# Kernel tuning notes

Measured on AMD Instinct MI355X. Metric: run time of the kernel, lower is better.

## Reference

```python
import jax, jax.numpy as jnp
import numpy as np

B, C_IN, N_NODES = 128, 64, 1024
N_TRIPLES = 3 * (N_NODES - 1)  # node 0 is the shared zero vector


def _btc(x, idx, w, b):
    # x: [B, C, N]; idx: [B, 3M]; w: [O, C, 3]; b: [O]
    Bv, C, _ = x.shape
    T = idx.shape[1]
    g = jnp.take_along_axis(x, jnp.broadcast_to(idx[:, None, :], (Bv, C, T)), axis=2)
    g = g.reshape(Bv, C, T // 3, 3)  # stride-3 kernel-3 conv == per-triple contraction
    out = jnp.einsum('bcnk,ock->bon', g, w) + b[None, :, None]
    zero = jnp.zeros((Bv, out.shape[1], 1), dtype=out.dtype)
    return jnp.concatenate([zero, out], axis=2)  # re-prepend zero node -> [B, O, N]


def _tln(x):
    mean = jnp.mean(x, axis=(1, 2), keepdims=True)
    std = jnp.std(x, axis=(1, 2), ddof=1, keepdims=True)  # torch.std is unbiased
    return (x - mean) / (std + 1e-5)


def _tower(x, idx, p):
    x = jax.nn.leaky_relu(_tln(_btc(x, idx, p['w_conv1'], p['b_conv1'])), 0.01)
    x = jax.nn.leaky_relu(_tln(_btc(x, idx, p['w_conv2'], p['b_conv2'])), 0.01)
    x = _tln(_btc(x, idx, p['w_conv3'], p['b_conv3']))
    x = jnp.max(x, axis=2)  # DynamicPooling -> [B, 64]
    x = jax.nn.leaky_relu(x @ p['w_fc1'].T + p['b_fc1'], 0.01)
    return x @ p['w_fc2'].T + p['b_fc2']  # [B, 1]  (Dropout is identity at eval)


def setup_inputs() -> dict:
    key = jax.random.key(0)
    ks = jax.random.split(key, 12)
    s = 0.05
    return {
        'data1': jax.random.normal(ks[0], (B, C_IN, N_NODES), jnp.float32),
        'idx1': jax.random.randint(ks[1], (B, N_TRIPLES, 1), 0, N_NODES, dtype=jnp.int64)
                if jax.config.jax_enable_x64 else
                jax.random.randint(ks[1], (B, N_TRIPLES, 1), 0, N_NODES).astype(jnp.int32),
        'data2': jax.random.normal(ks[2], (B, C_IN, N_NODES), jnp.float32),
        'idx2': jax.random.randint(ks[3], (B, N_TRIPLES, 1), 0, N_NODES).astype(jnp.int32),
        'w_conv1': jax.random.normal(ks[4], (256, C_IN, 3), jnp.float32) * s,
        'b_conv1': jnp.zeros((256,), jnp.float32),
        'w_conv2': jax.random.normal(ks[5], (128, 256, 3), jnp.float32) * s,
        'b_conv2': jnp.zeros((128,), jnp.float32),
        'w_conv3': jax.random.normal(ks[6], (64, 128, 3), jnp.float32) * s,
        'b_conv3': jnp.zeros((64,), jnp.float32),
        'w_fc1': jax.random.normal(ks[7], (32, 64), jnp.float32) * s,
        'b_fc1': jnp.zeros((32,), jnp.float32),
        'w_fc2': jax.random.normal(ks[8], (1, 32), jnp.float32) * s,
        'b_fc2': jnp.zeros((1,), jnp.float32),
    }


def reference(data1, idx1, data2, idx2,
              w_conv1, b_conv1, w_conv2, b_conv2, w_conv3, b_conv3,
              w_fc1, b_fc1, w_fc2, b_fc2):
    p = dict(w_conv1=w_conv1, b_conv1=b_conv1, w_conv2=w_conv2, b_conv2=b_conv2,
             w_conv3=w_conv3, b_conv3=b_conv3, w_fc1=w_fc1, b_fc1=b_fc1,
             w_fc2=w_fc2, b_fc2=b_fc2)
    y1 = _tower(data1, idx1[..., 0], p)
    y2 = _tower(data2, idx2[..., 0], p)
    return jnp.squeeze(jax.nn.sigmoid(y1 - y2), axis=1)  # [B]
```

## Files before the change

### kernel.cpp

```cpp
#include <hip/hip_runtime.h>
#include <math.h>

typedef __attribute__((ext_vector_type(8))) short short8;
typedef __attribute__((ext_vector_type(4))) float f32x4;
typedef __attribute__((ext_vector_type(2))) float f32x2;

#define LRELU(x) ((x) > 0.0f ? (x) : 0.01f * (x))

struct __align__(4) Int3 { int x, y, z; };

__device__ __forceinline__ unsigned short f2bf(float f) {
    unsigned int u = __float_as_uint(f);
    return (unsigned short)((u + 0x7FFFu + ((u >> 16) & 1u)) >> 16);
}
__device__ __forceinline__ unsigned int pack_bf16_pair(float lo, float hi) {
    unsigned int ul = __float_as_uint(lo) + 0x8000u;
    unsigned int uh = __float_as_uint(hi) + 0x8000u;
    return (ul >> 16) | (uh & 0xFFFF0000u);
}
__device__ __forceinline__ float2 stats_from(const float* sums, int b, float count) {
    float s = sums[2 * b], q = sums[2 * b + 1];
    float mean = s / count;
    float var = (q - s * s / count) / (count - 1.0f);
    var = fmaxf(var, 0.0f);
    return make_float2(mean, 1.0f / (sqrtf(var) + 1e-5f));
}
__device__ __forceinline__ void atomicMaxF(float* a, float v) {
    if (v >= 0.0f) atomicMax((int*)a, __float_as_int(v));
    else           atomicMin((unsigned int*)a, __float_as_uint(v));
}
__device__ __forceinline__ unsigned int fp8x4_nact(unsigned int u, float a, float c) {
    f32x2 lo = __builtin_amdgcn_cvt_pk_f32_fp8(u, false);
    f32x2 hi = __builtin_amdgcn_cvt_pk_f32_fp8(u, true);
    lo = lo * a + c; hi = hi * a + c;
    f32x2 ml = lo * 0.01f, mh = hi * 0.01f;
    lo = __builtin_elementwise_max(lo, ml);
    hi = __builtin_elementwise_max(hi, mh);
    int r = __builtin_amdgcn_cvt_pk_fp8_f32(lo.x, lo.y, 0, false);
    r = __builtin_amdgcn_cvt_pk_fp8_f32(hi.x, hi.y, r, true);
    return (unsigned int)r;
}

template <int MT, int WM>
__device__ __forceinline__ void mfma_step(const unsigned short* wt, const unsigned short* gt,
                                          f32x4 (&acc)[MT][4],
                                          int wo, int wn, int quad, int l15, int blkid)
{
#pragma unroll
    for (int st = 0; st < 2; ++st) {
        short8 af[MT], bfv[4];
        const int qb = st * 4 + quad;
#pragma unroll
        for (int i = 0; i < MT; i++) {
            const int orow = wo * WM + i * 16 + l15;
            af[i] = *(const short8*)&wt[orow * 64 + ((qb ^ blkid) << 3)];
        }
#pragma unroll
        for (int t = 0; t < 4; t++) {
            const int nrow = wn * 64 + t * 16 + l15;
            bfv[t] = *(const short8*)&gt[nrow * 64 + ((qb ^ blkid) << 3)];
        }
#pragma unroll
        for (int i = 0; i < MT; i++)
#pragma unroll
            for (int t = 0; t < 4; t++)
                acc[i][t] = __builtin_amdgcn_mfma_f32_16x16x32_bf16(
                    af[i], bfv[t], acc[i][t], 0, 0, 0);
    }
}

__global__ void prep_all(const float* __restrict__ w1, unsigned short* __restrict__ wq1,
                         const float* __restrict__ w2, unsigned char* __restrict__ wq2,
                         const float* __restrict__ w3, unsigned char* __restrict__ wq3)
{
    const int tid = blockIdx.x * blockDim.x + threadIdx.x;
    const int stride = gridDim.x * blockDim.x;
    for (int i = tid; i < 256 * 192; i += stride) {
        int o = i / 192, kp = i - o * 192;
        int j = kp >> 6, c = kp & 63;
        wq1[i] = f2bf(w1[(o * 64 + c) * 3 + j]);
    }
    for (int i = tid; i < (128 * 768) >> 2; i += stride) {
        const int e0 = i << 2;
        const int o = e0 / 768, kp0 = e0 - o * 768;
        const int j = kp0 >> 8, c0 = kp0 & 255;
        const float* src = &w2[(o * 256 + c0) * 3 + j];
        float f0 = src[0], f1 = src[3], f2 = src[6], f3 = src[9];
        int r = __builtin_amdgcn_cvt_pk_fp8_f32(f0, f1, 0, false);
        r = __builtin_amdgcn_cvt_pk_fp8_f32(f2, f3, r, true);
        *(unsigned int*)&wq2[e0] = (unsigned int)r;
    }
    for (int i = tid; i < (64 * 384) >> 2; i += stride) {
        const int e0 = i << 2;
        const int o = e0 / 384, kp0 = e0 - o * 384;
        const int j = kp0 >> 7, c0 = kp0 & 127;
        const float* src = &w3[(o * 128 + c0) * 3 + j];
        float f0 = src[0], f1 = src[3], f2 = src[6], f3 = src[9];
        int r = __builtin_amdgcn_cvt_pk_fp8_f32(f0, f1, 0, false);
        r = __builtin_amdgcn_cvt_pk_fp8_f32(f2, f3, r, true);
        *(unsigned int*)&wq3[e0] = (unsigned int)r;
    }
}

__global__ __launch_bounds__(256) void transpose_in(const float* __restrict__ inA,
                                                    const float* __restrict__ inB,
                                                    unsigned short* __restrict__ xT,
                                                    float* __restrict__ sums,
                                                    unsigned int* __restrict__ pmax)
{
    const int b = blockIdx.y, n0 = blockIdx.x * 64;
    const float* in = (b >= 128 ? inB : inA) + ((size_t)(b & 127) * 64) * 1024;
    const int tid = threadIdx.x;
    if (blockIdx.x == 0 && blockIdx.y == 0) {
        const int nBv = gridDim.y;
        for (int i = tid; i < 3 * nBv * 2; i += 256) sums[i] = 0.0f;
        for (int i = tid; i < nBv * 64; i += 256) pmax[i] = 0xFFFFFFFFu;
    }
    __shared__ float tile[64][65];
    const int nn = tid & 63, cw = tid >> 6;
#pragma unroll
    for (int i = 0; i < 16; i++) {
        int c = i * 4 + cw;
        tile[c][nn] = in[(size_t)c * 1024 + n0 + nn];
    }
    __syncthreads();
    const int n = tid >> 2, cp = (tid & 3) * 16;
    unsigned int pk[8];
#pragma unroll
    for (int i = 0; i < 8; i++) {
        unsigned short lo = f2bf(tile[cp + 2 * i][n]);
        unsigned short hi = f2bf(tile[cp + 2 * i + 1][n]);
        pk[i] = (unsigned int)lo | ((unsigned int)hi << 16);
    }
    unsigned short* dst = xT + ((size_t)b * 1024 + n0 + n) * 64 + cp;
    uint4 v0 = {pk[0], pk[1], pk[2], pk[3]};
    uint4 v1 = {pk[4], pk[5], pk[6], pk[7]};
    *(uint4*)dst = v0;
    *(uint4*)(dst + 8) = v1;
}

__global__ __launch_bounds__(256) void norm_act_fp8(unsigned char* __restrict__ a,
                                                    const float* __restrict__ sums,
                                                    float count, int u4PerB)
{
    const int b = blockIdx.y;
    float2 st = stats_from(sums, b, count);
    const float na = st.y, nc = -st.x * st.y;
    uint4* p = (uint4*)a + (size_t)b * u4PerB;
    for (int idx = blockIdx.x * 256 + threadIdx.x; idx < u4PerB; idx += gridDim.x * 256) {
        uint4 v = p[idx];
        v.x = fp8x4_nact(v.x, na, nc);
        v.y = fp8x4_nact(v.y, na, nc);
        v.z = fp8x4_nact(v.z, na, nc);
        v.w = fp8x4_nact(v.w, na, nc);
        p[idx] = v;
    }
}

__global__ __launch_bounds__(256, 3) void conv1_mfma(
    const unsigned short* __restrict__ xT,
    const int* __restrict__ idxA,
    const int* __restrict__ idxB,
    const unsigned short* __restrict__ wq,
    const float* __restrict__ bias,
    unsigned char* __restrict__ out,
    float* __restrict__ sums)
{
    const int b   = blockIdx.x;
    const int o0  = blockIdx.y * 128;
    const int nt0 = blockIdx.z << 7;
    const int tid = threadIdx.x;
    const int lane = tid & 63, wave = tid >> 6;
    const int wo = wave & 1, wn = wave >> 1;
    const int quad = lane >> 4, l15 = lane & 15;
    const int blkid = lane & 7;

    __shared__ __align__(16) unsigned short wt[128 * 64];
    __shared__ __align__(16) unsigned short gt[128 * 64];

    f32x4 acc[4][4];
#pragma unroll
    for (int i = 0; i < 4; i++)
#pragma unroll
        for (int t = 0; t < 4; t++) acc[i][t] = (f32x4){0.f, 0.f, 0.f, 0.f};

    const unsigned short* xTb = xT + (((size_t)b) << 10) * 64;
    const int* idxb = (b >= 128 ? idxB : idxA) + (size_t)(b & 127) * 3069;

    const int gr = tid >> 1, gh = tid & 1;
    int s0, s1, s2;
    {
        int n = nt0 + gr;
        int t0 = (n == 0) ? 0 : (n - 1);
        const Int3 sv = *(const Int3*)&idxb[3 * t0];
        s0 = sv.x; s1 = sv.y; s2 = sv.z;
    }
    const int wr = tid >> 1, wseg = tid & 1;
    const unsigned short* wrow = wq + (size_t)(o0 + wr) * 192 + wseg * 32;
    const int gswz = gr & 7, wswz = wr & 7;

    uint4 g0A, g1A, g2A, g3A;
    uint4 g0B, g1B, g2B, g3B;

#define LOADC(S, KC) {                                                           \
        const int src_ = ((KC) == 0) ? s0 : (((KC) == 1) ? s1 : s2);             \
        const uint4* gp_ = (const uint4*)(xTb + (size_t)src_ * 64 + gh * 32);    \
        g0##S = gp_[0]; g1##S = gp_[1]; g2##S = gp_[2]; g3##S = gp_[3];          \
    }

#define STAGE(S, KC) {                                                           \
        const uint4* wp_ = (const uint4*)(wrow + ((KC) << 6));                   \
        uint4 wv0 = wp_[0], wv1 = wp_[1], wv2 = wp_[2], wv3 = wp_[3];            \
        *(uint4*)&gt[gr * 64 + (((gh << 2) | 0) ^ gswz) * 8] = g0##S;            \
        *(uint4*)&gt[gr * 64 + (((gh << 2) | 1) ^ gswz) * 8] = g1##S;            \
        *(uint4*)&gt[gr * 64 + (((gh << 2) | 2) ^ gswz) * 8] = g2##S;            \
        *(uint4*)&gt[gr * 64 + (((gh << 2) | 3) ^ gswz) * 8] = g3##S;            \
        *(uint4*)&wt[wr * 64 + ((wseg * 4 + 0) ^ wswz) * 8] = wv0;               \
        *(uint4*)&wt[wr * 64 + ((wseg * 4 + 1) ^ wswz) * 8] = wv1;               \
        *(uint4*)&wt[wr * 64 + ((wseg * 4 + 2) ^ wswz) * 8] = wv2;               \
        *(uint4*)&wt[wr * 64 + ((wseg * 4 + 3) ^ wswz) * 8] = wv3;               \
    }

    LOADC(A, 0);
    LOADC(B, 1);
    int kc = 0;
    for (; kc + 2 <= 3; kc += 2) {
        if (kc) __syncthreads();
        STAGE(A, kc);
        if (kc + 2 < 3) LOADC(A, kc + 2);
        __syncthreads();
        mfma_step<4, 64>(wt, gt, acc, wo, wn, quad, l15, blkid);
        __syncthreads();
        STAGE(B, kc + 1);
        __syncthreads();
        mfma_step<4, 64>(wt, gt, acc, wo, wn, quad, l15, blkid);
    }
    {
        __syncthreads();
        STAGE(A, 2);
        __syncthreads();
        mfma_step<4, 64>(wt, gt, acc, wo, wn, quad, l15, blkid);
    }
#undef LOADC
#undef STAGE

    __syncthreads();
    unsigned char* eb = (unsigned char*)gt;
    float lsum = 0.f, lsq = 0.f;
#pragma unroll
    for (int i = 0; i < 4; i++) {
        const int obl = wo * 64 + i * 16 + quad * 4;
        const float4 bv = *(const float4*)(bias + o0 + obl);
#pragma unroll
        for (int t = 0; t < 4; t++) {
            const int nl = wn * 64 + t * 16 + l15;
            float v0 = acc[i][t][0] + bv.x;
            float v1 = acc[i][t][1] + bv.y;
            float v2 = acc[i][t][2] + bv.z;
            float v3 = acc[i][t][3] + bv.w;
            if (nt0 + nl == 0) { v0 = v1 = v2 = v3 = 0.f; }
            lsum += v0 + v1 + v2 + v3;
            lsq  += v0 * v0 + v1 * v1 + v2 * v2 + v3 * v3;
            int r = __builtin_amdgcn_cvt_pk_fp8_f32(v0, v1, 0, false);
            r = __builtin_amdgcn_cvt_pk_fp8_f32(v2, v3, r, true);
            *(unsigned int*)&eb[nl * 128 + (obl ^ ((nl & 7) << 4))] = (unsigned int)r;
        }
    }
#pragma unroll
    for (int off = 32; off > 0; off >>= 1) {
        lsum += __shfl_down(lsum, off);
        lsq  += __shfl_down(lsq, off);
    }
    float* red = (float*)wt;
    if (lane == 0) { red[wave] = lsum; red[4 + wave] = lsq; }
    __syncthreads();
#pragma unroll
    for (int c = 0; c < 4; ++c) {
        const int ch = c * 256 + tid;
        const int row = ch >> 3, off = (ch & 7) << 4;
        uint4 v = *(const uint4*)&eb[row * 128 + (off ^ ((row & 7) << 4))];
        *(uint4*)&out[((size_t)b * 1024 + nt0 + row) * 256 + o0 + off] = v;
    }
    if (tid == 0) {
        atomicAdd(&sums[2 * b + 0], red[0] + red[1] + red[2] + red[3]);
        atomicAdd(&sums[2 * b + 1], red[4] + red[5] + red[6] + red[7]);
    }
}

__global__ __launch_bounds__(256, 3) void conv2_fp8(
    const unsigned char* __restrict__ a1,
    const int* __restrict__ idxA,
    const int* __restrict__ idxB,
    const unsigned char* __restrict__ wq8,
    const float* __restrict__ bias,
    unsigned char* __restrict__ out,
    float* __restrict__ sums)
{
    const int b   = blockIdx.x;
    const int nt0 = blockIdx.z << 7;
    const int tid = threadIdx.x;
    const int lane = tid & 63, wave = tid >> 6;
    const int wo = wave & 1, wn = wave >> 1;
    const int quad = lane >> 4, l15 = lane & 15;
    const int blkid = lane & 7;

    __shared__ __align__(16) unsigned char wt8[128 * 128];
    __shared__ __align__(16) unsigned char gt8[128 * 128];

    f32x4 acc[4][4];
#pragma unroll
    for (int i = 0; i < 4; i++)
#pragma unroll
        for (int t = 0; t < 4; t++) acc[i][t] = (f32x4){0.f, 0.f, 0.f, 0.f};

    const unsigned char* xb = a1 + (((size_t)b) << 10) * 256;
    const int* idxb = (b >= 128 ? idxB : idxA) + (size_t)(b & 127) * 3069;

    const int gr = tid >> 1, gh = tid & 1;
    int si0, si1, si2;
    {
        int n = nt0 + gr;
        int t0 = (n == 0) ? 0 : (n - 1);
        const Int3 sv = *(const Int3*)&idxb[3 * t0];
        si0 = sv.x; si1 = sv.y; si2 = sv.z;
    }
    const unsigned char* wrow = wq8 + (size_t)gr * 768 + gh * 64;
    const int swz = gr & 7;

    uint4 g0A, g1A, g2A, g3A;
    uint4 g0B, g1B, g2B, g3B;

#define LOADC2(S, KC) {                                                          \
        const int j_  = (KC) >> 1;                                               \
        const int c0_ = ((KC) & 1) << 7;                                         \
        const int src_ = (j_ == 0) ? si0 : ((j_ == 1) ? si1 : si2);              \
        const uint4* gp_ = (const uint4*)(xb + (size_t)src_ * 256 + c0_ + gh * 64); \
        g0##S = gp_[0]; g1##S = gp_[1]; g2##S = gp_[2]; g3##S = gp_[3];          \
    }

#define STAGE2(S, KC) {                                                          \
        const uint4* wp_ = (const uint4*)(wrow + (KC) * 128);                    \
        uint4 wv0 = wp_[0], wv1 = wp_[1], wv2 = wp_[2], wv3 = wp_[3];            \
        *(uint4*)&gt8[gr * 128 + (((gh << 2) | 0) ^ swz) * 16] = g0##S;          \
        *(uint4*)&gt8[gr * 128 + (((gh << 2) | 1) ^ swz) * 16] = g1##S;          \
        *(uint4*)&gt8[gr * 128 + (((gh << 2) | 2) ^ swz) * 16] = g2##S;          \
        *(uint4*)&gt8[gr * 128 + (((gh << 2) | 3) ^ swz) * 16] = g3##S;          \
        *(uint4*)&wt8[gr * 128 + (((gh << 2) | 0) ^ swz) * 16] = wv0;            \
        *(uint4*)&wt8[gr * 128 + (((gh << 2) | 1) ^ swz) * 16] = wv1;            \
        *(uint4*)&wt8[gr * 128 + (((gh << 2) | 2) ^ swz) * 16] = wv2;            \
        *(uint4*)&wt8[gr * 128 + (((gh << 2) | 3) ^ swz) * 16] = wv3;            \
    }

#define MFMA_STEP2 {                                                             \
        _Pragma("unroll")                                                        \
        for (int st = 0; st < 4; ++st) {                                         \
            long af0, af1, af2, af3, bf0, bf1, bf2, bf3;                         \
            const int qb = st * 4 + quad;                                        \
            const int cg = qb >> 1, ch = (qb & 1) << 3;                          \
            {                                                                    \
                const int r0 = wo * 64 + 0 * 16 + l15;                           \
                af0 = *(const long*)&wt8[r0 * 128 + ((cg ^ blkid) << 4) + ch];   \
                const int r1 = wo * 64 + 1 * 16 + l15;                           \
                af1 = *(const long*)&wt8[r1 * 128 + ((cg ^ blkid) << 4) + ch];   \
                const int r2 = wo * 64 + 2 * 16 + l15;                           \
                af2 = *(const long*)&wt8[r2 * 128 + ((cg ^ blkid) << 4) + ch];   \
                const int r3 = wo * 64 + 3 * 16 + l15;                           \
                af3 = *(const long*)&wt8[r3 * 128 + ((cg ^ blkid) << 4) + ch];   \
                const int n0 = wn * 64 + 0 * 16 + l15;                           \
                bf0 = *(const long*)&gt8[n0 * 128 + ((cg ^ blkid) << 4) + ch];   \
                const int n1 = wn * 64 + 1 * 16 + l15;                           \
                bf1 = *(const long*)&gt8[n1 * 128 + ((cg ^ blkid) << 4) + ch];   \
                const int n2 = wn * 64 + 2 * 16 + l15;                           \
                bf2 = *(const long*)&gt8[n2 * 128 + ((cg ^ blkid) << 4) + ch];   \
                const int n3 = wn * 64 + 3 * 16 + l15;                           \
                bf3 = *(const long*)&gt8[n3 * 128 + ((cg ^ blkid) << 4) + ch];   \
            }                                                                    \
            acc[0][0] = __builtin_amdgcn_mfma_f32_16x16x32_fp8_fp8(af0, bf0, acc[0][0], 0, 0, 0); \
            acc[0][1] = __builtin_amdgcn_mfma_f32_16x16x32_fp8_fp8(af0, bf1, acc[0][1], 0, 0, 0); \
            acc[0][2] = __builtin_amdgcn_mfma_f32_16x16x32_fp8_fp8(af0, bf2, acc[0][2], 0, 0, 0); \
            acc[0][3] = __builtin_amdgcn_mfma_f32_16x16x32_fp8_fp8(af0, bf3, acc[0][3], 0, 0, 0); \
            acc[1][0] = __builtin_amdgcn_mfma_f32_16x16x32_fp8_fp8(af1, bf0, acc[1][0], 0, 0, 0); \
            acc[1][1] = __builtin_amdgcn_mfma_f32_16x16x32_fp8_fp8(af1, bf1, acc[1][1], 0, 0, 0); \
            acc[1][2] = __builtin_amdgcn_mfma_f32_16x16x32_fp8_fp8(af1, bf2, acc[1][2], 0, 0, 0); \
            acc[1][3] = __builtin_amdgcn_mfma_f32_16x16x32_fp8_fp8(af1, bf3, acc[1][3], 0, 0, 0); \
            acc[2][0] = __builtin_amdgcn_mfma_f32_16x16x32_fp8_fp8(af2, bf0, acc[2][0], 0, 0, 0); \
            acc[2][1] = __builtin_amdgcn_mfma_f32_16x16x32_fp8_fp8(af2, bf1, acc[2][1], 0, 0, 0); \
            acc[2][2] = __builtin_amdgcn_mfma_f32_16x16x32_fp8_fp8(af2, bf2, acc[2][2], 0, 0, 0); \
            acc[2][3] = __builtin_amdgcn_mfma_f32_16x16x32_fp8_fp8(af2, bf3, acc[2][3], 0, 0, 0); \
            acc[3][0] = __builtin_amdgcn_mfma_f32_16x16x32_fp8_fp8(af3, bf0, acc[3][0], 0, 0, 0); \
            acc[3][1] = __builtin_amdgcn_mfma_f32_16x16x32_fp8_fp8(af3, bf1, acc[3][1], 0, 0, 0); \
            acc[3][2] = __builtin_amdgcn_mfma_f32_16x16x32_fp8_fp8(af3, bf2, acc[3][2], 0, 0, 0); \
            acc[3][3] = __builtin_amdgcn_mfma_f32_16x16x32_fp8_fp8(af3, bf3, acc[3][3], 0, 0, 0); \
        }                                                                        \
    }

    LOADC2(A, 0);
    LOADC2(B, 1);
    int kc = 0;
    for (; kc + 2 <= 6; kc += 2) {
        if (kc) __syncthreads();
        STAGE2(A, kc);
        if (kc + 2 < 6) LOADC2(A, kc + 2);
        __syncthreads();
        MFMA_STEP2;
        __syncthreads();
        STAGE2(B, kc + 1);
        if (kc + 3 < 6) LOADC2(B, kc + 3);
        __syncthreads();
        MFMA_STEP2;
    }
#undef LOADC2
#undef STAGE2
#undef MFMA_STEP2

    __syncthreads();
    unsigned char* eb = gt8;
    float lsum = 0.f, lsq = 0.f;
#pragma unroll
    for (int i = 0; i < 4; i++) {
        const int obl = wo * 64 + i * 16 + quad * 4;
        const float4 bv = *(const float4*)(bias + obl);
#pragma unroll
        for (int t = 0; t < 4; t++) {
            const int nl = wn * 64 + t * 16 + l15;
            float v0 = acc[i][t][0] + bv.x;
            float v1 = acc[i][t][1] + bv.y;
            float v2 = acc[i][t][2] + bv.z;
            float v3 = acc[i][t][3] + bv.w;
            if (nt0 + nl == 0) { v0 = v1 = v2 = v3 = 0.f; }
            lsum += v0 + v1 + v2 + v3;
            lsq  += v0 * v0 + v1 * v1 + v2 * v2 + v3 * v3;
            int r = __builtin_amdgcn_cvt_pk_fp8_f32(v0, v1, 0, false);
            r = __builtin_amdgcn_cvt_pk_fp8_f32(v2, v3, r, true);
            *(unsigned int*)&eb[nl * 128 + (obl ^ ((nl & 7) << 4))] = (unsigned int)r;
        }
    }
#pragma unroll
    for (int off = 32; off > 0; off >>= 1) {
        lsum += __shfl_down(lsum, off);
        lsq  += __shfl_down(lsq, off);
    }
    float* red = (float*)wt8;
    if (lane == 0) { red[wave] = lsum; red[4 + wave] = lsq; }
    __syncthreads();
#pragma unroll
    for (int c = 0; c < 4; ++c) {
        const int ch = c * 256 + tid;
        const int row = ch >> 3, off = (ch & 7) << 4;
        uint4 v = *(const uint4*)&eb[row * 128 + (off ^ ((row & 7) << 4))];
        *(uint4*)&out[((size_t)b * 1024 + nt0 + row) * 128 + off] = v;
    }
    if (tid == 0) {
        atomicAdd(&sums[2 * b + 0], red[0] + red[1] + red[2] + red[3]);
        atomicAdd(&sums[2 * b + 1], red[4] + red[5] + red[6] + red[7]);
    }
}

__global__ __launch_bounds__(256, 3) void conv3_fp8(
    const unsigned char* __restrict__ a2,
    const int* __restrict__ idxA,
    const int* __restrict__ idxB,
    const unsigned char* __restrict__ wq8,
    const float* __restrict__ bias,
    float* __restrict__ sums,
    float* __restrict__ pmax)
{
    const int b   = blockIdx.x;
    const int nt0 = blockIdx.z << 7;
    const int tid = threadIdx.x;
    const int lane = tid & 63, wave = tid >> 6;
    const int wo = wave & 1, wn = wave >> 1;
    const int quad = lane >> 4, l15 = lane & 15;
    const int blkid = lane & 7;

    __shared__ __align__(16) unsigned char wt8[64 * 128];
    __shared__ __align__(16) unsigned char gt8[128 * 128];

    f32x4 acc[2][4];
#pragma unroll
    for (int i = 0; i < 2; i++)
#pragma unroll
        for (int t = 0; t < 4; t++) acc[i][t] = (f32x4){0.f, 0.f, 0.f, 0.f};

    const unsigned char* xb = a2 + (((size_t)b) << 10) * 128;
    const int* idxb = (b >= 128 ? idxB : idxA) + (size_t)(b & 127) * 3069;

    const int gr = tid >> 1, gh = tid & 1;
    int si0, si1, si2;
    {
        int n = nt0 + gr;
        int t0 = (n == 0) ? 0 : (n - 1);
        const Int3 sv = *(const Int3*)&idxb[3 * t0];
        si0 = sv.x; si1 = sv.y; si2 = sv.z;
    }
    const int wr = tid >> 2, wseg = tid & 3;
    const unsigned char* wrow = wq8 + (size_t)wr * 384 + wseg * 32;
    const int gswz = gr & 7, wswz = wr & 7;

    uint4 g0A, g1A, g2A, g3A;
    uint4 g0B, g1B, g2B, g3B;

#define LOADC3(S, KC) {                                                          \
        const int src_ = ((KC) == 0) ? si0 : (((KC) == 1) ? si1 : si2);          \
        const uint4* gp_ = (const uint4*)(xb + (size_t)src_ * 128 + gh * 64);    \
        g0##S = gp_[0]; g1##S = gp_[1]; g2##S = gp_[2]; g3##S = gp_[3];          \
    }

#define STAGE3(S, KC) {                                                          \
        const uint4* wp_ = (const uint4*)(wrow + (KC) * 128);                    \
        uint4 wv0 = wp_[0], wv1 = wp_[1];                                        \
        *(uint4*)&gt8[gr * 128 + (((gh << 2) | 0) ^ gswz) * 16] = g0##S;         \
        *(uint4*)&gt8[gr * 128 + (((gh << 2) | 1) ^ gswz) * 16] = g1##S;         \
        *(uint4*)&gt8[gr * 128 + (((gh << 2) | 2) ^ gswz) * 16] = g2##S;         \
        *(uint4*)&gt8[gr * 128 + (((gh << 2) | 3) ^ gswz) * 16] = g3##S;         \
        *(uint4*)&wt8[wr * 128 + (((wseg << 1) | 0) ^ wswz) * 16] = wv0;         \
        *(uint4*)&wt8[wr * 128 + (((wseg << 1) | 1) ^ wswz) * 16] = wv1;         \
    }

#define MFMA_STEP3 {                                                             \
        _Pragma("unroll")                                                        \
        for (int st = 0; st < 4; ++st) {                                         \
            long af0, af1, bf0, bf1, bf2, bf3;                                   \
            const int qb = st * 4 + quad;                                        \
            const int cg = qb >> 1, ch = (qb & 1) << 3;                          \
            {                                                                    \
                const int r0 = wo * 32 + 0 * 16 + l15;                           \
                af0 = *(const long*)&wt8[r0 * 128 + ((cg ^ blkid) << 4) + ch];   \
                const int r1 = wo * 32 + 1 * 16 + l15;                           \
                af1 = *(const long*)&wt8[r1 * 128 + ((cg ^ blkid) << 4) + ch];   \
                const int n0 = wn * 64 + 0 * 16 + l15;                           \
                bf0 = *(const long*)&gt8[n0 * 128 + ((cg ^ blkid) << 4) + ch];   \
                const int n1 = wn * 64 + 1 * 16 + l15;                           \
                bf1 = *(const long*)&gt8[n1 * 128 + ((cg ^ blkid) << 4) + ch];   \
                const int n2 = wn * 64 + 2 * 16 + l15;                           \
                bf2 = *(const long*)&gt8[n2 * 128 + ((cg ^ blkid) << 4) + ch];   \
                const int n3 = wn * 64 + 3 * 16 + l15;                           \
                bf3 = *(const long*)&gt8[n3 * 128 + ((cg ^ blkid) << 4) + ch];   \
            }                                                                    \
            acc[0][0] = __builtin_amdgcn_mfma_f32_16x16x32_fp8_fp8(af0, bf0, acc[0][0], 0, 0, 0); \
            acc[0][1] = __builtin_amdgcn_mfma_f32_16x16x32_fp8_fp8(af0, bf1, acc[0][1], 0, 0, 0); \
            acc[0][2] = __builtin_amdgcn_mfma_f32_16x16x32_fp8_fp8(af0, bf2, acc[0][2], 0, 0, 0); \
            acc[0][3] = __builtin_amdgcn_mfma_f32_16x16x32_fp8_fp8(af0, bf3, acc[0][3], 0, 0, 0); \
            acc[1][0] = __builtin_amdgcn_mfma_f32_16x16x32_fp8_fp8(af1, bf0, acc[1][0], 0, 0, 0); \
            acc[1][1] = __builtin_amdgcn_mfma_f32_16x16x32_fp8_fp8(af1, bf1, acc[1][1], 0, 0, 0); \
            acc[1][2] = __builtin_amdgcn_mfma_f32_16x16x32_fp8_fp8(af1, bf2, acc[1][2], 0, 0, 0); \
            acc[1][3] = __builtin_amdgcn_mfma_f32_16x16x32_fp8_fp8(af1, bf3, acc[1][3], 0, 0, 0); \
        }                                                                        \
    }

    LOADC3(A, 0);
    LOADC3(B, 1);
    int kc = 0;
    for (; kc + 2 <= 3; kc += 2) {
        if (kc) __syncthreads();
        STAGE3(A, kc);
        if (kc + 2 < 3) LOADC3(A, kc + 2);
        __syncthreads();
        MFMA_STEP3;
        __syncthreads();
        STAGE3(B, kc + 1);
        __syncthreads();
        MFMA_STEP3;
    }
    {
        __syncthreads();
        STAGE3(A, 2);
        __syncthreads();
        MFMA_STEP3;
    }
#undef LOADC3
#undef STAGE3
#undef MFMA_STEP3

    __syncthreads();
    float lsum = 0.f, lsq = 0.f;
#pragma unroll
    for (int i = 0; i < 2; i++) {
        const int ob = wo * 32 + i * 16 + quad * 4;
        const float4 bv = *(const float4*)(bias + ob);
        float mx0 = -1e30f, mx1 = -1e30f, mx2 = -1e30f, mx3 = -1e30f;
#pragma unroll
        for (int t = 0; t < 4; t++) {
            const int n = nt0 + wn * 64 + t * 16 + l15;
            float v0 = acc[i][t][0] + bv.x;
            float v1 = acc[i][t][1] + bv.y;
            float v2 = acc[i][t][2] + bv.z;
            float v3 = acc[i][t][3] + bv.w;
            if (n == 0) { v0 = v1 = v2 = v3 = 0.f; }
            lsum += v0 + v1 + v2 + v3;
            lsq  += v0 * v0 + v1 * v1 + v2 * v2 + v3 * v3;
            mx0 = fmaxf(mx0, v0); mx1 = fmaxf(mx1, v1);
            mx2 = fmaxf(mx2, v2); mx3 = fmaxf(mx3, v3);
        }
#pragma unroll
        for (int off = 1; off < 16; off <<= 1) {
            mx0 = fmaxf(mx0, __shfl_xor(mx0, off));
            mx1 = fmaxf(mx1, __shfl_xor(mx1, off));
            mx2 = fmaxf(mx2, __shfl_xor(mx2, off));
            mx3 = fmaxf(mx3, __shfl_xor(mx3, off));
        }
        if (l15 == 0) {
            atomicMaxF(&pmax[(size_t)b * 64 + ob + 0], mx0);
            atomicMaxF(&pmax[(size_t)b * 64 + ob + 1], mx1);
            atomicMaxF(&pmax[(size_t)b * 64 + ob + 2], mx2);
            atomicMaxF(&pmax[(size_t)b * 64 + ob + 3], mx3);
        }
    }
#pragma unroll
    for (int off = 32; off > 0; off >>= 1) {
        lsum += __shfl_down(lsum, off);
        lsq  += __shfl_down(lsq, off);
    }
    float* red = (float*)wt8;
    if (lane == 0) { red[wave] = lsum; red[4 + wave] = lsq; }
    __syncthreads();
    if (tid == 0) {
        atomicAdd(&sums[2 * b + 0], red[0] + red[1] + red[2] + red[3]);
        atomicAdd(&sums[2 * b + 1], red[4] + red[5] + red[6] + red[7]);
    }
}

__global__ __launch_bounds__(64) void fc_head(
    const float* __restrict__ pmax, const float* __restrict__ sums3, float count,
    const float* __restrict__ w_fc1, const float* __restrict__ b_fc1,
    const float* __restrict__ w_fc2, const float* __restrict__ b_fc2,
    float* __restrict__ y)
{
    const int b = blockIdx.x, t = threadIdx.x;
    __shared__ float pooled[64];
    __shared__ float hid[32];
    float2 s = stats_from(sums3, b, count);
    pooled[t] = (pmax[(size_t)b * 64 + t] - s.x) * s.y;
    __syncthreads();
    if (t < 32) {
        float h = b_fc1[t];
#pragma unroll
        for (int c = 0; c < 64; c++) h += pooled[c] * w_fc1[t * 64 + c];
        hid[t] = LRELU(h);
    }
    __syncthreads();
    if (t == 0) {
        float v = b_fc2[0];
#pragma unroll
        for (int c = 0; c < 32; c++) v += hid[c] * w_fc2[c];
        y[b] = v;
    }
}

__global__ void sigmoid_diff(const float* __restrict__ y1,
                             const float* __restrict__ y2,
                             float* __restrict__ out)
{
    int b = threadIdx.x;
    if (b < 128) out[b] = 1.0f / (1.0f + expf(-(y1[b] - y2[b])));
}

extern "C" void kernel_launch(void* const* d_in, const int* in_sizes, int n_in,
                              void* d_out, int out_size, void* d_ws, size_t ws_size,
                              hipStream_t stream)
{
    const float* data1 = (const float*)d_in[0];
    const int*   idx1  = (const int*)d_in[1];
    const float* data2 = (const float*)d_in[2];
    const int*   idx2  = (const int*)d_in[3];
    const float* w1 = (const float*)d_in[4];
    const float* b1 = (const float*)d_in[5];
    const float* w2 = (const float*)d_in[6];
    const float* b2 = (const float*)d_in[7];
    const float* w3 = (const float*)d_in[8];
    const float* b3 = (const float*)d_in[9];
    const float* wfc1 = (const float*)d_in[10];
    const float* bfc1 = (const float*)d_in[11];
    const float* wfc2 = (const float*)d_in[12];
    const float* bfc2 = (const float*)d_in[13];

    const size_t needM = (size_t)256 * 1024 * (64 * 2 + 256 * 1 + 128 * 1) + 768 * 1024;
    const bool merged = ws_size >= needM;
    const int nB = merged ? 256 : 128;
    const size_t szXT = (size_t)nB * 1024 * 64 * 2;
    const size_t szA1 = (size_t)nB * 1024 * 256;
    const size_t szA2 = (size_t)nB * 1024 * 128;

    char* ws = (char*)d_ws;
    unsigned short* xT = (unsigned short*)ws;
    unsigned char*  a1 = (unsigned char*)(ws + szXT);
    unsigned char*  a2 = (unsigned char*)(ws + szXT + szA1);
    char* tail = ws + szXT + szA1 + szA2;
    unsigned short* wq1   = (unsigned short*)tail;
    unsigned char*  wq2f8 = (unsigned char*)(tail + 128 * 1024);
    unsigned char*  wq3f8 = (unsigned char*)(tail + 384 * 1024);
    float* sums = (float*)(tail + 448 * 1024);
    float* pmax = (float*)(tail + 512 * 1024);
    float* yv   = (float*)(tail + 640 * 1024);

    prep_all<<<96, 256, 0, stream>>>(w1, wq1, w2, wq2f8, w3, wq3f8);

    const int nIter = merged ? 1 : 2;
    for (int t = 0; t < nIter; ++t) {
        const float* dA = (merged || t == 0) ? data1 : data2;
        const float* dB = merged ? data2 : dA;
        const int* iA = (merged || t == 0) ? idx1 : idx2;
        const int* iB = merged ? idx2 : iA;
        float* s1 = sums;
        float* s2 = sums + nB * 2;
        float* s3 = sums + nB * 4;

        transpose_in<<<dim3(16, nB), 256, 0, stream>>>(dA, dB, xT, sums,
                                                       (unsigned int*)pmax);

        conv1_mfma<<<dim3(nB, 2, 8), 256, 0, stream>>>(
            xT, iA, iB, wq1, b1, a1, s1);

        norm_act_fp8<<<dim3(16, nB), 256, 0, stream>>>(a1, s1, 256.0f * 1024.0f, 16384);

        conv2_fp8<<<dim3(nB, 1, 8), 256, 0, stream>>>(
            a1, iA, iB, wq2f8, b2, a2, s2);

        norm_act_fp8<<<dim3(8, nB), 256, 0, stream>>>(a2, s2, 128.0f * 1024.0f, 8192);

        conv3_fp8<<<dim3(nB, 1, 8), 256, 0, stream>>>(
            a2, iA, iB, wq3f8, b3, s3, pmax);

        fc_head<<<nB, 64, 0, stream>>>(pmax, s3, 64.0f * 1024.0f,
                                       wfc1, bfc1, wfc2, bfc2,
                                       yv + (merged ? 0 : t * 128));
    }
    sigmoid_diff<<<1, 128, 0, stream>>>(yv, yv + 128, (float*)d_out);
}
```

Before: 281.6 us.

## Permute fp8 K layout so MFMA fragments load as 16-byte LDS reads

Reorders the K dimension of the fp8 weights (in prep) and of the conv1/conv2 epilogue outputs (via perm128) so each lane's two consecutive K-steps sit in one contiguous 16-byte chunk. The conv2/conv3 MFMA inner loops then issue half as many, wider LDS reads (ulonglong2 instead of two 8-byte longs). This targets LDS instruction count and latency in the fp8 GEMM stages. The permutation must match exactly across the weights, the activation writes and the gather/stage code, otherwise results are silently wrong.

Measured after the change: 269.5 us. -4.3%, faster.

```diff
diff --git a/kernel.cpp b/kernel.cpp
--- a/kernel.cpp
+++ b/kernel.cpp
@@ -40,6 +40,9 @@
     r = __builtin_amdgcn_cvt_pk_fp8_f32(hi.x, hi.y, r, true);
     return (unsigned int)r;
 }
+__device__ __forceinline__ int perm128(int o) {
+    return ((o >> 6) << 6) | (((o >> 3) & 3) << 4) | (((o >> 5) & 1) << 3) | (o & 7);
+}
 
 template <int MT, int WM>
 __device__ __forceinline__ void mfma_step(const unsigned short* wt, const unsigned short* gt,
@@ -82,7 +85,10 @@
     }
     for (int i = tid; i < (128 * 768) >> 2; i += stride) {
         const int e0 = i << 2;
-        const int o = e0 / 768, kp0 = e0 - o * 768;
+        const int o = e0 / 768, r0 = e0 - o * 768;
+        const int kc = r0 >> 7, ro = r0 & 127;
+        const int k0 = ((ro >> 6) << 6) + (((ro >> 3) & 1) << 5) + (((ro >> 4) & 3) << 3) + (ro & 7);
+        const int kp0 = kc * 128 + k0;
         const int j = kp0 >> 8, c0 = kp0 & 255;
         const float* src = &w2[(o * 256 + c0) * 3 + j];
         float f0 = src[0], f1 = src[3], f2 = src[6], f3 = src[9];
@@ -92,7 +98,10 @@
     }
     for (int i = tid; i < (64 * 384) >> 2; i += stride) {
         const int e0 = i << 2;
-        const int o = e0 / 384, kp0 = e0 - o * 384;
+        const int o = e0 / 384, r0 = e0 - o * 384;
+        const int kc = r0 >> 7, ro = r0 & 127;
+        const int k0 = ((ro >> 6) << 6) + (((ro >> 3) & 1) << 5) + (((ro >> 4) & 3) << 3) + (ro & 7);
+        const int kp0 = kc * 128 + k0;
         const int j = kp0 >> 7, c0 = kp0 & 127;
         const float* src = &w3[(o * 128 + c0) * 3 + j];
         float f0 = src[0], f1 = src[3], f2 = src[6], f3 = src[9];
@@ -250,6 +259,7 @@
 #pragma unroll
     for (int i = 0; i < 4; i++) {
         const int obl = wo * 64 + i * 16 + quad * 4;
+        const int op  = perm128(obl);
         const float4 bv = *(const float4*)(bias + o0 + obl);
 #pragma unroll
         for (int t = 0; t < 4; t++) {
@@ -263,7 +273,7 @@
             lsq  += v0 * v0 + v1 * v1 + v2 * v2 + v3 * v3;
             int r = __builtin_amdgcn_cvt_pk_fp8_f32(v0, v1, 0, false);
             r = __builtin_amdgcn_cvt_pk_fp8_f32(v2, v3, r, true);
-            *(unsigned int*)&eb[nl * 128 + (obl ^ ((nl & 7) << 4))] = (unsigned int)r;
+            *(unsigned int*)&eb[nl * 128 + (op ^ ((nl & 7) << 4))] = (unsigned int)r;
         }
     }
 #pragma unroll
@@ -353,44 +363,51 @@
 
 #define MFMA_STEP2 {                                                             \
         _Pragma("unroll")                                                        \
-        for (int st = 0; st < 4; ++st) {                                         \
-            long af0, af1, af2, af3, bf0, bf1, bf2, bf3;                         \
-            const int qb = st * 4 + quad;                                        \
-            const int cg = qb >> 1, ch = (qb & 1) << 3;                          \
+        for (int pp = 0; pp < 2; ++pp) {                                         \
+            ulonglong2 a0v, a1v, a2v, a3v, b0v, b1v, b2v, b3v;                   \
             {                                                                    \
-                const int r0 = wo * 64 + 0 * 16 + l15;                           \
-                af0 = *(const long*)&wt8[r0 * 128 + ((cg ^ blkid) << 4) + ch];   \
-                const int r1 = wo * 64 + 1 * 16 + l15;                           \
-                af1 = *(const long*)&wt8[r1 * 128 + ((cg ^ blkid) << 4) + ch];   \
-                const int r2 = wo * 64 + 2 * 16 + l15;                           \
-                af2 = *(const long*)&wt8[r2 * 128 + ((cg ^ blkid) << 4) + ch];   \
-                const int r3 = wo * 64 + 3 * 16 + l15;                           \
-                af3 = *(const long*)&wt8[r3 * 128 + ((cg ^ blkid) << 4) + ch];   \
-                const int n0 = wn * 64 + 0 * 16 + l15;                           \
-                bf0 = *(const long*)&gt8[n0 * 128 + ((cg ^ blkid) << 4) + ch];   \
-                const int n1 = wn * 64 + 1 * 16 + l15;                           \
-                bf1 = *(const long*)&gt8[n1 * 128 + ((cg ^ blkid) << 4) + ch];   \
-                const int n2 = wn * 64 + 2 * 16 + l15;                           \
-                bf2 = *(const long*)&gt8[n2 * 128 + ((cg ^ blkid) << 4) + ch];   \
-                const int n3 = wn * 64 + 3 * 16 + l15;                           \
-                bf3 = *(const long*)&gt8[n3 * 128 + ((cg ^ blkid) << 4) + ch];   \
+                const int cx = (((pp * 4 + quad) ^ blkid) << 4);                 \
+                a0v = *(const ulonglong2*)&wt8[(wo * 64 +  0 + l15) * 128 + cx]; \
+                a1v = *(const ulonglong2*)&wt8[(wo * 64 + 16 + l15) * 128 + cx]; \
+                a2v = *(const ulonglong2*)&wt8[(wo * 64 + 32 + l15) * 128 + cx]; \
+                a3v = *(const ulonglong2*)&wt8[(wo * 64 + 48 + l15) * 128 + cx]; \
+                b0v = *(const ulonglong2*)&gt8[(wn * 64 +  0 + l15) * 128 + cx]; \
+                b1v = *(const ulonglong2*)&gt8[(wn * 64 + 16 + l15) * 128 + cx]; \
+                b2v = *(const ulonglong2*)&gt8[(wn * 64 + 32 + l15) * 128 + cx]; \
+                b3v = *(const ulonglong2*)&gt8[(wn * 64 + 48 + l15) * 128 + cx]; \
             }                                                                    \
-            acc[0][0] = __builtin_amdgcn_mfma_f32_16x16x32_fp8_fp8(af0, bf0, acc[0][0], 0, 0, 0); \
-            acc[0][1] = __builtin_amdgcn_mfma_f32_16x16x32_fp8_fp8(af0, bf1, acc[0][1], 0, 0, 0); \
-            acc[0][2] = __builtin_amdgcn_mfma_f32_16x16x32_fp8_fp8(af0, bf2, acc[0][2], 0, 0, 0); \
-            acc[0][3] = __builtin_amdgcn_mfma_f32_16x16x32_fp8_fp8(af0, bf3, acc[0][3], 0, 0, 0); \
-            acc[1][0] = __builtin_amdgcn_mfma_f32_16x16x32_fp8_fp8(af1, bf0, acc[1][0], 0, 0, 0); \
-            acc[1][1] = __builtin_amdgcn_mfma_f32_16x16x32_fp8_fp8(af1, bf1, acc[1][1], 0, 0, 0); \
-            acc[1][2] = __builtin_amdgcn_mfma_f32_16x16x32_fp8_fp8(af1, bf2, acc[1][2], 0, 0, 0); \
-            acc[1][3] = __builtin_amdgcn_mfma_f32_16x16x32_fp8_fp8(af1, bf3, acc[1][3], 0, 0, 0); \
-            acc[2][0] = __builtin_amdgcn_mfma_f32_16x16x32_fp8_fp8(af2, bf0, acc[2][0], 0, 0, 0); \
-            acc[2][1] = __builtin_amdgcn_mfma_f32_16x16x32_fp8_fp8(af2, bf1, acc[2][1], 0, 0, 0); \
-            acc[2][2] = __builtin_amdgcn_mfma_f32_16x16x32_fp8_fp8(af2, bf2, acc[2][2], 0, 0, 0); \
-            acc[2][3] = __builtin_amdgcn_mfma_f32_16x16x32_fp8_fp8(af2, bf3, acc[2][3], 0, 0, 0); \
-            acc[3][0] = __builtin_amdgcn_mfma_f32_16x16x32_fp8_fp8(af3, bf0, acc[3][0], 0, 0, 0); \
-            acc[3][1] = __builtin_amdgcn_mfma_f32_16x16x32_fp8_fp8(af3, bf1, acc[3][1], 0, 0, 0); \
-            acc[3][2] = __builtin_amdgcn_mfma_f32_16x16x32_fp8_fp8(af3, bf2, acc[3][2], 0, 0, 0); \
-            acc[3][3] = __builtin_amdgcn_mfma_f32_16x16x32_fp8_fp8(af3, bf3, acc[3][3], 0, 0, 0); \
+            acc[0][0] = __builtin_amdgcn_mfma_f32_16x16x32_fp8_fp8((long)a0v.x, (long)b0v.x, acc[0][0], 0, 0, 0); \
+            acc[0][1] = __builtin_amdgcn_mfma_f32_16x16x32_fp8_fp8((long)a0v.x, (long)b1v.x, acc[0][1], 0, 0, 0); \
+            acc[0][2] = __builtin_amdgcn_mfma_f32_16x16x32_fp8_fp8((long)a0v.x, (long)b2v.x, acc[0][2], 0, 0, 0); \
+            acc[0][3] = __builtin_amdgcn_mfma_f32_16x16x32_fp8_fp8((long)a0v.x, (long)b3v.x, acc[0][3], 0, 0, 0); \
+            acc[1][0] = __builtin_amdgcn_mfma_f32_16x16x32_fp8_fp8((long)a1v.x, (long)b0v.x, acc[1][0], 0, 0, 0); \
+            acc[1][1] = __builtin_amdgcn_mfma_f32_16x16x32_fp8_fp8((long)a1v.x, (long)b1v.x, acc[1][1], 0, 0, 0); \
+            acc[1][2] = __builtin_amdgcn_mfma_f32_16x16x32_fp8_fp8((long)a1v.x, (long)b2v.x, acc[1][2], 0, 0, 0); \
+            acc[1][3] = __builtin_amdgcn_mfma_f32_16x16x32_fp8_fp8((long)a1v.x, (long)b3v.x, acc[1][3], 0, 0, 0); \
+            acc[2][0] = __builtin_amdgcn_mfma_f32_16x16x32_fp8_fp8((long)a2v.x, (long)b0v.x, acc[2][0], 0, 0, 0); \
+            acc[2][1] = __builtin_amdgcn_mfma_f32_16x16x32_fp8_fp8((long)a2v.x, (long)b1v.x, acc[2][1], 0, 0, 0); \
+            acc[2][2] = __builtin_amdgcn_mfma_f32_16x16x32_fp8_fp8((long)a2v.x, (long)b2v.x, acc[2][2], 0, 0, 0); \
+            acc[2][3] = __builtin_amdgcn_mfma_f32_16x16x32_fp8_fp8((long)a2v.x, (long)b3v.x, acc[2][3], 0, 0, 0); \
+            acc[3][0] = __builtin_amdgcn_mfma_f32_16x16x32_fp8_fp8((long)a3v.x, (long)b0v.x, acc[3][0], 0, 0, 0); \
+            acc[3][1] = __builtin_amdgcn_mfma_f32_16x16x32_fp8_fp8((long)a3v.x, (long)b1v.x, acc[3][1], 0, 0, 0); \
+            acc[3][2] = __builtin_amdgcn_mfma_f32_16x16x32_fp8_fp8((long)a3v.x, (long)b2v.x, acc[3][2], 0, 0, 0); \
+            acc[3][3] = __builtin_amdgcn_mfma_f32_16x16x32_fp8_fp8((long)a3v.x, (long)b3v.x, acc[3][3], 0, 0, 0); \
+            acc[0][0] = __builtin_amdgcn_mfma_f32_16x16x32_fp8_fp8((long)a0v.y, (long)b0v.y, acc[0][0], 0, 0, 0); \
+            acc[0][1] = __builtin_amdgcn_mfma_f32_16x16x32_fp8_fp8((long)a0v.y, (long)b1v.y, acc[0][1], 0, 0, 0); \
+            acc[0][2] = __builtin_amdgcn_mfma_f32_16x16x32_fp8_fp8((long)a0v.y, (long)b2v.y, acc[0][2], 0, 0, 0); \
+            acc[0][3] = __builtin_amdgcn_mfma_f32_16x16x32_fp8_fp8((long)a0v.y, (long)b3v.y, acc[0][3], 0, 0, 0); \
+            acc[1][0] = __builtin_amdgcn_mfma_f32_16x16x32_fp8_fp8((long)a1v.y, (long)b0v.y, acc[1][0], 0, 0, 0); \
+            acc[1][1] = __builtin_amdgcn_mfma_f32_16x16x32_fp8_fp8((long)a1v.y, (long)b1v.y, acc[1][1], 0, 0, 0); \
+            acc[1][2] = __builtin_amdgcn_mfma_f32_16x16x32_fp8_fp8((long)a1v.y, (long)b2v.y, acc[1][2], 0, 0, 0); \
+            acc[1][3] = __builtin_amdgcn_mfma_f32_16x16x32_fp8_fp8((long)a1v.y, (long)b3v.y, acc[1][3], 0, 0, 0); \
+            acc[2][0] = __builtin_amdgcn_mfma_f32_16x16x32_fp8_fp8((long)a2v.y, (long)b0v.y, acc[2][0], 0, 0, 0); \
+            acc[2][1] = __builtin_amdgcn_mfma_f32_16x16x32_fp8_fp8((long)a2v.y, (long)b1v.y, acc[2][1], 0, 0, 0); \
+            acc[2][2] = __builtin_amdgcn_mfma_f32_16x16x32_fp8_fp8((long)a2v.y, (long)b2v.y, acc[2][2], 0, 0, 0); \
+            acc[2][3] = __builtin_amdgcn_mfma_f32_16x16x32_fp8_fp8((long)a2v.y, (long)b3v.y, acc[2][3], 0, 0, 0); \
+            acc[3][0] = __builtin_amdgcn_mfma_f32_16x16x32_fp8_fp8((long)a3v.y, (long)b0v.y, acc[3][0], 0, 0, 0); \
+            acc[3][1] = __builtin_amdgcn_mfma_f32_16x16x32_fp8_fp8((long)a3v.y, (long)b1v.y, acc[3][1], 0, 0, 0); \
+            acc[3][2] = __builtin_amdgcn_mfma_f32_16x16x32_fp8_fp8((long)a3v.y, (long)b2v.y, acc[3][2], 0, 0, 0); \
+            acc[3][3] = __builtin_amdgcn_mfma_f32_16x16x32_fp8_fp8((long)a3v.y, (long)b3v.y, acc[3][3], 0, 0, 0); \
         }                                                                        \
     }
 
@@ -419,6 +436,7 @@
 #pragma unroll
     for (int i = 0; i < 4; i++) {
         const int obl = wo * 64 + i * 16 + quad * 4;
+        const int op  = perm128(obl);
         const float4 bv = *(const float4*)(bias + obl);
 #pragma unroll
         for (int t = 0; t < 4; t++) {
@@ -432,7 +450,7 @@
             lsq  += v0 * v0 + v1 * v1 + v2 * v2 + v3 * v3;
             int r = __builtin_amdgcn_cvt_pk_fp8_f32(v0, v1, 0, false);
             r = __builtin_amdgcn_cvt_pk_fp8_f32(v2, v3, r, true);
-            *(unsigned int*)&eb[nl * 128 + (obl ^ ((nl & 7) << 4))] = (unsigned int)r;
+            *(unsigned int*)&eb[nl * 128 + (op ^ ((nl & 7) << 4))] = (unsigned int)r;
         }
     }
 #pragma unroll
@@ -519,32 +537,33 @@
 
 #define MFMA_STEP3 {                                                             \
         _Pragma("unroll")                                                        \
-        for (int st = 0; st < 4; ++st) {                                         \
-            long af0, af1, bf0, bf1, bf2, bf3;                                   \
-            const int qb = st * 4 + quad;                                        \
-            const int cg = qb >> 1, ch = (qb & 1) << 3;                          \
+        for (int pp = 0; pp < 2; ++pp) {                                         \
+            ulonglong2 a0v, a1v, b0v, b1v, b2v, b3v;                             \
             {                                                                    \
-                const int r0 = wo * 32 + 0 * 16 + l15;                           \
-                af0 = *(const long*)&wt8[r0 * 128 + ((cg ^ blkid) << 4) + ch];   \
-                const int r1 = wo * 32 + 1 * 16 + l15;                           \
-                af1 = *(const long*)&wt8[r1 * 128 + ((cg ^ blkid) << 4) + ch];   \
-                const int n0 = wn * 64 + 0 * 16 + l15;                           \
-                bf0 = *(const long*)&gt8[n0 * 128 + ((cg ^ blkid) << 4) + ch];   \
-                const int n1 = wn * 64 + 1 * 16 + l15;                           \
-                bf1 = *(const long*)&gt8[n1 * 128 + ((cg ^ blkid) << 4) + ch];   \
-                const int n2 = wn * 64 + 2 * 16 + l15;                           \
-                bf2 = *(const long*)&gt8[n2 * 128 + ((cg ^ blkid) << 4) + ch];   \
-                const int n3 = wn * 64 + 3 * 16 + l15;                           \
-                bf3 = *(const long*)&gt8[n3 * 128 + ((cg ^ blkid) << 4) + ch];   \
+                const int cx = (((pp * 4 + quad) ^ blkid) << 4);                 \
+                a0v = *(const ulonglong2*)&wt8[(wo * 32 +  0 + l15) * 128 + cx]; \
+                a1v = *(const ulonglong2*)&wt8[(wo * 32 + 16 + l15) * 128 + cx]; \
+                b0v = *(const ulonglong2*)&gt8[(wn * 64 +  0 + l15) * 128 + cx]; \
+                b1v = *(const ulonglong2*)&gt8[(wn * 64 + 16 + l15) * 128 + cx]; \
+                b2v = *(const ulonglong2*)&gt8[(wn * 64 + 32 + l15) * 128 + cx]; \
+                b3v = *(const ulonglong2*)&gt8[(wn * 64 + 48 + l15) * 128 + cx]; \
             }                                                                    \
-            acc[0][0] = __builtin_amdgcn_mfma_f32_16x16x32_fp8_fp8(af0, bf0, acc[0][0], 0, 0, 0); \
-            acc[0][1] = __builtin_amdgcn_mfma_f32_16x16x32_fp8_fp8(af0, bf1, acc[0][1], 0, 0, 0); \
-            acc[0][2] = __builtin_amdgcn_mfma_f32_16x16x32_fp8_fp8(af0, bf2, acc[0][2], 0, 0, 0); \
-            acc[0][3] = __builtin_amdgcn_mfma_f32_16x16x32_fp8_fp8(af0, bf3, acc[0][3], 0, 0, 0); \
-            acc[1][0] = __builtin_amdgcn_mfma_f32_16x16x32_fp8_fp8(af1, bf0, acc[1][0], 0, 0, 0); \
-            acc[1][1] = __builtin_amdgcn_mfma_f32_16x16x32_fp8_fp8(af1, bf1, acc[1][1], 0, 0, 0); \
-            acc[1][2] = __builtin_amdgcn_mfma_f32_16x16x32_fp8_fp8(af1, bf2, acc[1][2], 0, 0, 0); \
-            acc[1][3] = __builtin_amdgcn_mfma_f32_16x16x32_fp8_fp8(af1, bf3, acc[1][3], 0, 0, 0); \
+            acc[0][0] = __builtin_amdgcn_mfma_f32_16x16x32_fp8_fp8((long)a0v.x, (long)b0v.x, acc[0][0], 0, 0, 0); \
+            acc[0][1] = __builtin_amdgcn_mfma_f32_16x16x32_fp8_fp8((long)a0v.x, (long)b1v.x, acc[0][1], 0, 0, 0); \
+            acc[0][2] = __builtin_amdgcn_mfma_f32_16x16x32_fp8_fp8((long)a0v.x, (long)b2v.x, acc[0][2], 0, 0, 0); \
+            acc[0][3] = __builtin_amdgcn_mfma_f32_16x16x32_fp8_fp8((long)a0v.x, (long)b3v.x, acc[0][3], 0, 0, 0); \
+            acc[1][0] = __builtin_amdgcn_mfma_f32_16x16x32_fp8_fp8((long)a1v.x, (long)b0v.x, acc[1][0], 0, 0, 0); \
+            acc[1][1] = __builtin_amdgcn_mfma_f32_16x16x32_fp8_fp8((long)a1v.x, (long)b1v.x, acc[1][1], 0, 0, 0); \
+            acc[1][2] = __builtin_amdgcn_mfma_f32_16x16x32_fp8_fp8((long)a1v.x, (long)b2v.x, acc[1][2], 0, 0, 0); \
+            acc[1][3] = __builtin_amdgcn_mfma_f32_16x16x32_fp8_fp8((long)a1v.x, (long)b3v.x, acc[1][3], 0, 0, 0); \
+            acc[0][0] = __builtin_amdgcn_mfma_f32_16x16x32_fp8_fp8((long)a0v.y, (long)b0v.y, acc[0][0], 0, 0, 0); \
+            acc[0][1] = __builtin_amdgcn_mfma_f32_16x16x32_fp8_fp8((long)a0v.y, (long)b1v.y, acc[0][1], 0, 0, 0); \
+            acc[0][2] = __builtin_amdgcn_mfma_f32_16x16x32_fp8_fp8((long)a0v.y, (long)b2v.y, acc[0][2], 0, 0, 0); \
+            acc[0][3] = __builtin_amdgcn_mfma_f32_16x16x32_fp8_fp8((long)a0v.y, (long)b3v.y, acc[0][3], 0, 0, 0); \
+            acc[1][0] = __builtin_amdgcn_mfma_f32_16x16x32_fp8_fp8((long)a1v.y, (long)b0v.y, acc[1][0], 0, 0, 0); \
+            acc[1][1] = __builtin_amdgcn_mfma_f32_16x16x32_fp8_fp8((long)a1v.y, (long)b1v.y, acc[1][1], 0, 0, 0); \
+            acc[1][2] = __builtin_amdgcn_mfma_f32_16x16x32_fp8_fp8((long)a1v.y, (long)b2v.y, acc[1][2], 0, 0, 0); \
+            acc[1][3] = __builtin_amdgcn_mfma_f32_16x16x32_fp8_fp8((long)a1v.y, (long)b3v.y, acc[1][3], 0, 0, 0); \
         }                                                                        \
     }
 
```
